# Kernel optimization log

Measured on AMD Instinct MI355X. Metric: run time of the kernel, lower is better.

Reference implementation:

```python
import jax, jax.numpy as jnp
import numpy as np

# Dimensions
B, T, S, V, CV, D = 32, 128, 400, 32000, 600, 512
PAD = 1  # vocabs['code'].stoi['<blank>']


def setup_inputs() -> dict:
    key = jax.random.key(0)
    k0, k1, k2, k3, k4 = jax.random.split(key, 5)
    hidden = jax.random.normal(k0, (B * T, D), dtype=jnp.float32)
    # attention weights: normalized over source length
    copy_attn = jax.nn.softmax(jax.random.normal(k1, (B * T, S), dtype=jnp.float32), axis=-1)
    # src_map: one-hot scatter matrix [B, S, CV] mapping src positions to extended-vocab ids
    src_ids = jax.random.randint(k2, (B, S), 0, CV)
    src_map = jax.nn.one_hot(src_ids, CV, dtype=jnp.float32)
    W = jax.random.normal(k3, (V, D), dtype=jnp.float32) * 0.02
    b = jnp.zeros((V,), dtype=jnp.float32)
    w_copy = jax.random.normal(k4, (D,), dtype=jnp.float32) * 0.02
    b_copy = jnp.zeros((), dtype=jnp.float32)
    return {"hidden": hidden, "copy_attn": copy_attn, "src_map": src_map,
            "W": W, "b": b, "w_copy": w_copy, "b_copy": b_copy}


def reference(hidden, copy_attn, src_map, W, b, w_copy, b_copy):
    # logits over target vocab, pad logit masked to -inf
    logits = hidden @ W.T + b                      # [B*T, V]
    logits = logits.at[:, PAD].set(-jnp.inf)
    prob = jax.nn.softmax(logits, axis=-1)         # [B*T, V]
    # copy gate p(z)
    copy = jax.nn.sigmoid(hidden @ w_copy + b_copy)[:, None]  # [B*T, 1]
    out_prob = prob * (1.0 - copy)                 # generation branch
    mul_attn = copy_attn * copy                    # copy branch, [B*T, S]
    # scatter attention mass into extended vocab via one-hot bmm
    copy_prob = jnp.einsum('bts,bsv->btv', mul_attn.reshape(B, T, S), src_map)
    copy_prob = copy_prob.reshape(-1, src_map.shape[-1])  # [B*T, CV]
    return jnp.concatenate([out_prob, copy_prob], axis=1)  # [B*T, V+CV]
```

## Files before the change

### kernel.cpp

```cpp
#include <hip/hip_runtime.h>
#include <hip/hip_bf16.h>
#include <cstdint>
#include <cstddef>

#define M_ROWS   4096
#define N_VOCAB  32000
#define K_DIM    512
#define S_DIM    400
#define CV_DIM   600
#define OUT_PITCH 32600
#define PAD_IDX  1

typedef __attribute__((ext_vector_type(8))) short short8;
typedef __attribute__((ext_vector_type(8))) unsigned short ushort8;
typedef __attribute__((ext_vector_type(4))) float f32x4;

#define WB_OFF   0ull
#define HB_OFF   32768000ull
#define COPYG_OFF 36962304ull
#define RSUM_OFF  36978688ull
#define SSCALE_OFF 36995072ull
#define SRCID_OFF 37011456ull
#define EB_OFF    37062656ull
#define WS_NEED_BF16 (EB_OFF + 262144000ull)

__device__ inline void gload_lds16(const void* g, void* l) {
  __builtin_amdgcn_global_load_lds(
      (const __attribute__((address_space(1))) unsigned int*)g,
      (__attribute__((address_space(3))) unsigned int*)l, 16, 0, 0);
}

__device__ inline unsigned short f32_to_bf16_rn(float f) {
  unsigned u = __float_as_uint(f);
  u += 0x7FFFu + ((u >> 16) & 1u);
  return (unsigned short)(u >> 16);
}
__device__ inline float bf16_to_f32(unsigned short h) {
  return __uint_as_float((unsigned)h << 16);
}

__global__ void cvt_kernel(const float4* __restrict__ in, ushort4* __restrict__ out, unsigned n4) {
  unsigned stride = gridDim.x * blockDim.x;
  for (unsigned i = blockIdx.x * blockDim.x + threadIdx.x; i < n4; i += stride) {
    float4 v = in[i];
    ushort4 o;
    o.x = f32_to_bf16_rn(v.x);
    o.y = f32_to_bf16_rn(v.y);
    o.z = f32_to_bf16_rn(v.z);
    o.w = f32_to_bf16_rn(v.w);
    out[i] = o;
  }
}

__global__ void copygate_kernel(const float* __restrict__ hidden, const float* __restrict__ w_copy,
                                const float* __restrict__ b_copy, float* __restrict__ copyg) {
  unsigned gw = (blockIdx.x * blockDim.x + threadIdx.x) >> 6;
  unsigned lane = threadIdx.x & 63u;
  if (gw >= M_ROWS) return;
  const float4* h4 = (const float4*)(hidden + (size_t)gw * K_DIM);
  const float4* w4 = (const float4*)w_copy;
  float dot = 0.f;
  #pragma unroll
  for (int i = 0; i < 2; ++i) {
    float4 a = h4[lane * 2 + i], w = w4[lane * 2 + i];
    dot += a.x * w.x + a.y * w.y + a.z * w.z + a.w * w.w;
  }
  #pragma unroll
  for (int mask = 1; mask < 64; mask <<= 1) dot += __shfl_xor(dot, mask);
  if (lane == 0) copyg[gw] = 1.f / (1.f + __expf(-(dot + b_copy[0])));
}

__global__ void srcids_kernel(const float* __restrict__ src_map, int* __restrict__ src_ids) {
  unsigned pos = (blockIdx.x * blockDim.x + threadIdx.x) >> 6;
  unsigned lane = threadIdx.x & 63u;
  if (pos >= 32 * S_DIM) return;
  const float* row = src_map + (size_t)pos * CV_DIM;
  int found = 1 << 30;
  for (int v = lane; v < CV_DIM; v += 64)
    if (row[v] > 0.5f) found = v;
  #pragma unroll
  for (int mask = 1; mask < 64; mask <<= 1) {
    int o = __shfl_xor(found, mask);
    found = found < o ? found : o;
  }
  if (lane == 0) src_ids[pos] = found;
}

template<int BF16OUT>
__global__ __launch_bounds__(256, 4)
void gemm_exp_kernel(const unsigned short* __restrict__ A,
                     const unsigned short* __restrict__ B,
                     const float* __restrict__ bias,
                     float* __restrict__ out,
                     unsigned short* __restrict__ Eb,
                     float* __restrict__ row_sum) {
  __shared__ unsigned short smem[16384];
  unsigned short* As = smem;
  unsigned short* Bs = smem + 8192;

  unsigned bid = blockIdx.x;
  unsigned wg = (bid & 7u) * 1000u + (bid >> 3);
  unsigned mt = wg / 250u, nt = wg % 250u;
  unsigned m0 = mt * 128u, n0 = nt * 128u;
  unsigned tid = threadIdx.x;
  unsigned lane = tid & 63u;
  unsigned wid = tid >> 6;
  unsigned wm = wid >> 1, wn = wid & 1u;
  unsigned lr = lane >> 4, lc = lane & 15u;

  const unsigned ch0 = (lr ^ (lc & 7u)) * 8u;
  const unsigned ch1 = ((lr + 4u) ^ (lc & 7u)) * 8u;

  const unsigned short* Asrc[4];
  const unsigned short* Bsrc[4];
  unsigned dst[4];
  #pragma unroll
  for (unsigned i = 0; i < 4; ++i) {
    unsigned u = i * 256u + tid;
    unsigned rr = u >> 3;
    unsigned ch = (u & 7u) ^ (rr & 7u);
    dst[i] = u * 16u;
    Asrc[i] = A + (size_t)(m0 + rr) * K_DIM + ch * 8u;
    Bsrc[i] = B + (size_t)(n0 + rr) * K_DIM + ch * 8u;
  }
  unsigned arow[4], brow[4];
  #pragma unroll
  for (int m = 0; m < 4; ++m) arow[m] = (wm * 64u + m * 16u + lc) * 64u;
  #pragma unroll
  for (int n = 0; n < 4; ++n) brow[n] = (wn * 64u + n * 16u + lc) * 64u;

  f32x4 acc[4][4] = {};

  for (unsigned kt = 0; kt < 8; ++kt) {
    unsigned k0 = kt * 64u;
    #pragma unroll
    for (unsigned i = 0; i < 4; ++i) {
      gload_lds16(Asrc[i] + k0, (char*)As + dst[i]);
      gload_lds16(Bsrc[i] + k0, (char*)Bs + dst[i]);
    }
    __syncthreads();
    {
      short8 af[4][2], bf[4][2];
      #pragma unroll
      for (int m = 0; m < 4; ++m) {
        af[m][0] = *(const short8*)&As[arow[m] + ch0];
        af[m][1] = *(const short8*)&As[arow[m] + ch1];
      }
      #pragma unroll
      for (int n = 0; n < 4; ++n) {
        bf[n][0] = *(const short8*)&Bs[brow[n] + ch0];
        bf[n][1] = *(const short8*)&Bs[brow[n] + ch1];
      }
      #pragma unroll
      for (int ks = 0; ks < 2; ++ks)
        #pragma unroll
        for (int m = 0; m < 4; ++m)
          #pragma unroll
          for (int n = 0; n < 4; ++n)
            acc[m][n] = __builtin_amdgcn_mfma_f32_16x16x32_bf16(af[m][ks], bf[n][ks],
                                                                acc[m][n], 0, 0, 0);
    }
    __syncthreads();
  }

  float bv[4];
  #pragma unroll
  for (int n = 0; n < 4; ++n) bv[n] = bias[n0 + wn * 64u + n * 16u + lc];

  if (BF16OUT) {
    #pragma unroll
    for (int m = 0; m < 4; ++m)
      #pragma unroll
      for (int j = 0; j < 4; ++j) {
        unsigned r = wm * 64u + m * 16u + lr * 4u + j;
        #pragma unroll
        for (int n = 0; n < 4; ++n) {
          unsigned c = wn * 64u + n * 16u + lc;
          unsigned gcol = n0 + c;
          float e = (gcol == PAD_IDX) ? 0.f : __expf(acc[m][n][j] + bv[n]);
          smem[r * 128u + (c ^ ((r & 7u) << 3))] = f32_to_bf16_rn(e);
        }
      }
    __syncthreads();
    {
      unsigned r = tid >> 1, c0 = (tid & 1u) * 64u;
      unsigned short* gdst = Eb + (size_t)(m0 + r) * N_VOCAB + n0 + c0;
      #pragma unroll
      for (unsigned q = 0; q < 8; ++q) {
        ushort8 v = *(const ushort8*)&smem[r * 128u + c0 + ((q ^ (r & 7u)) << 3)];
        *(ushort8*)(gdst + q * 8u) = v;
      }
    }
  } else {
    #pragma unroll
    for (int m = 0; m < 4; ++m) {
      #pragma unroll
      for (int j = 0; j < 4; ++j) {
        unsigned grow = m0 + wm * 64u + m * 16u + lr * 4u + j;
        float rs = 0.f;
        #pragma unroll
        for (int n = 0; n < 4; ++n) {
          unsigned gcol = n0 + wn * 64u + n * 16u + lc;
          float e = (gcol == PAD_IDX) ? 0.f : __expf(acc[m][n][j] + bv[n]);
          out[(size_t)grow * OUT_PITCH + gcol] = e;
          rs += e;
        }
        #pragma unroll
        for (int mask = 1; mask < 16; mask <<= 1) rs += __shfl_xor(rs, mask);
        if (lc == 0) atomicAdd(&row_sum[grow], rs);
      }
    }
  }
}

__global__ __launch_bounds__(256)
void norm_scale_kernel(const unsigned short* __restrict__ Eb,
                       const float* __restrict__ copyg,
                       float* __restrict__ out) {
  unsigned r = blockIdx.x;
  unsigned tid = threadIdx.x;
  const ushort8* src = (const ushort8*)(Eb + (size_t)r * N_VOCAB);
  ushort8 v[16];
  float lsum = 0.f;
  #pragma unroll
  for (int i = 0; i < 16; ++i) {
    unsigned c = (unsigned)i * 256u + tid;
    if (c < 4000u) {
      v[i] = src[c];
      #pragma unroll
      for (int k = 0; k < 8; ++k) lsum += bf16_to_f32(v[i][k]);
    }
  }
  #pragma unroll
  for (int mask = 1; mask < 64; mask <<= 1) lsum += __shfl_xor(lsum, mask);
  __shared__ float wsum[4];
  if ((tid & 63u) == 0) wsum[tid >> 6] = lsum;
  __syncthreads();
  float s = (1.f - copyg[r]) / (wsum[0] + wsum[1] + wsum[2] + wsum[3]);
  float* dst = out + (size_t)r * OUT_PITCH;
  #pragma unroll
  for (int i = 0; i < 16; ++i) {
    unsigned c = (unsigned)i * 256u + tid;
    if (c < 4000u) {
      float4 lo, hi;
      lo.x = bf16_to_f32(v[i][0]) * s; lo.y = bf16_to_f32(v[i][1]) * s;
      lo.z = bf16_to_f32(v[i][2]) * s; lo.w = bf16_to_f32(v[i][3]) * s;
      hi.x = bf16_to_f32(v[i][4]) * s; hi.y = bf16_to_f32(v[i][5]) * s;
      hi.z = bf16_to_f32(v[i][6]) * s; hi.w = bf16_to_f32(v[i][7]) * s;
      float4* o = (float4*)(dst + c * 8u);
      o[0] = lo; o[1] = hi;
    }
  }
}

__global__ void finalize_kernel(const float* __restrict__ row_sum, const float* __restrict__ copyg,
                                float* __restrict__ sscale) {
  unsigned r = blockIdx.x * blockDim.x + threadIdx.x;
  if (r < M_ROWS) sscale[r] = (1.f - copyg[r]) / row_sum[r];
}

__global__ void scale_kernel(float4* __restrict__ out, const float* __restrict__ sscale) {
  const unsigned total = M_ROWS * (N_VOCAB / 4);
  unsigned stride = gridDim.x * blockDim.x;
  for (unsigned i = blockIdx.x * blockDim.x + threadIdx.x; i < total; i += stride) {
    unsigned r = i / (N_VOCAB / 4);
    unsigned c = i % (N_VOCAB / 4);
    float s = sscale[r];
    float4 v = out[(size_t)r * (OUT_PITCH / 4) + c];
    v.x *= s; v.y *= s; v.z *= s; v.w *= s;
    out[(size_t)r * (OUT_PITCH / 4) + c] = v;
  }
}

__global__ void copyprob_kernel(const float* __restrict__ attn, const int* __restrict__ src_ids,
                                const float* __restrict__ copyg, float* __restrict__ out) {
  unsigned r = blockIdx.x;
  unsigned tid = threadIdx.x;
  __shared__ float cp[CV_DIM];
  for (unsigned v = tid; v < CV_DIM; v += 128) cp[v] = 0.f;
  __syncthreads();
  unsigned batch = r >> 7;
  float g = copyg[r];
  for (unsigned s = tid; s < S_DIM; s += 128) {
    float a = attn[(size_t)r * S_DIM + s] * g;
    atomicAdd(&cp[src_ids[batch * S_DIM + s]], a);
  }
  __syncthreads();
  for (unsigned v = tid; v < CV_DIM; v += 128)
    out[(size_t)r * OUT_PITCH + N_VOCAB + v] = cp[v];
}

extern "C" void kernel_launch(void* const* d_in, const int* in_sizes, int n_in,
                              void* d_out, int out_size, void* d_ws, size_t ws_size,
                              hipStream_t stream) {
  const float* hidden    = (const float*)d_in[0];
  const float* copy_attn = (const float*)d_in[1];
  const float* src_map   = (const float*)d_in[2];
  const float* W         = (const float*)d_in[3];
  const float* bias      = (const float*)d_in[4];
  const float* w_copy    = (const float*)d_in[5];
  const float* b_copy    = (const float*)d_in[6];
  float* out = (float*)d_out;

  char* ws = (char*)d_ws;
  unsigned short* Wb = (unsigned short*)(ws + WB_OFF);
  unsigned short* Hb = (unsigned short*)(ws + HB_OFF);
  float* copyg   = (float*)(ws + COPYG_OFF);
  float* row_sum = (float*)(ws + RSUM_OFF);
  float* sscale  = (float*)(ws + SSCALE_OFF);
  int*   src_ids = (int*)(ws + SRCID_OFF);
  unsigned short* Eb = (unsigned short*)(ws + EB_OFF);

  const bool bf16_path = (ws_size >= WS_NEED_BF16);

  cvt_kernel<<<2048, 256, 0, stream>>>((const float4*)W, (ushort4*)Wb,
                                       (unsigned)(N_VOCAB * K_DIM / 4));
  cvt_kernel<<<1024, 256, 0, stream>>>((const float4*)hidden, (ushort4*)Hb,
                                       (unsigned)(M_ROWS * K_DIM / 4));
  copygate_kernel<<<M_ROWS / 4, 256, 0, stream>>>(hidden, w_copy, b_copy, copyg);
  srcids_kernel<<<(32 * S_DIM) / 4, 256, 0, stream>>>(src_map, src_ids);

  if (bf16_path) {
    gemm_exp_kernel<1><<<(M_ROWS / 128) * (N_VOCAB / 128), 256, 0, stream>>>(
        Hb, Wb, bias, out, Eb, row_sum);
    norm_scale_kernel<<<M_ROWS, 256, 0, stream>>>(Eb, copyg, out);
  } else {
    hipMemsetAsync(row_sum, 0, M_ROWS * sizeof(float), stream);
    gemm_exp_kernel<0><<<(M_ROWS / 128) * (N_VOCAB / 128), 256, 0, stream>>>(
        Hb, Wb, bias, out, Eb, row_sum);
    finalize_kernel<<<(M_ROWS + 255) / 256, 256, 0, stream>>>(row_sum, copyg, sscale);
    scale_kernel<<<4096, 256, 0, stream>>>((float4*)out, sscale);
  }

  copyprob_kernel<<<M_ROWS, 128, 0, stream>>>(copy_attn, src_ids, copyg, out);
}
```

Before: 431.3 us.

## Double-buffer GEMM K-loop with 32-wide K tiles and async prefetch

Rewrites the GEMM main loop to use two LDS buffers of 32-wide K tiles, so the global-to-LDS load for the next tile is issued before computing on the current one. Uses explicit vmcnt waits and raw s_barrier instead of __syncthreads, and adds a new XOR swizzle for the 4-chunk rows. This is meant to hide global load latency behind MFMA work. In exchange it runs twice as many loop iterations with more barriers, and its correctness depends on the manual waitcnt counts.

```diff
diff --git a/kernel.cpp b/kernel.cpp
--- a/kernel.cpp
+++ b/kernel.cpp
@@ -95,8 +95,6 @@
                      unsigned short* __restrict__ Eb,
                      float* __restrict__ row_sum) {
   __shared__ unsigned short smem[16384];
-  unsigned short* As = smem;
-  unsigned short* Bs = smem + 8192;
 
   unsigned bid = blockIdx.x;
   unsigned wg = (bid & 7u) * 1000u + (bid >> 3);
@@ -108,59 +106,66 @@
   unsigned wm = wid >> 1, wn = wid & 1u;
   unsigned lr = lane >> 4, lc = lane & 15u;
 
-  const unsigned ch0 = (lr ^ (lc & 7u)) * 8u;
-  const unsigned ch1 = ((lr + 4u) ^ (lc & 7u)) * 8u;
-
-  const unsigned short* Asrc[4];
-  const unsigned short* Bsrc[4];
-  unsigned dst[4];
-  #pragma unroll
-  for (unsigned i = 0; i < 4; ++i) {
+  const unsigned ch = lr ^ (lc & 3u) ^ ((lc >> 2) & 3u);
+
+  const unsigned short* AsrcP[2];
+  const unsigned short* BsrcP[2];
+  unsigned dstB[2];
+  #pragma unroll
+  for (unsigned i = 0; i < 2; ++i) {
     unsigned u = i * 256u + tid;
-    unsigned rr = u >> 3;
-    unsigned ch = (u & 7u) ^ (rr & 7u);
-    dst[i] = u * 16u;
-    Asrc[i] = A + (size_t)(m0 + rr) * K_DIM + ch * 8u;
-    Bsrc[i] = B + (size_t)(n0 + rr) * K_DIM + ch * 8u;
-  }
-  unsigned arow[4], brow[4];
-  #pragma unroll
-  for (int m = 0; m < 4; ++m) arow[m] = (wm * 64u + m * 16u + lc) * 64u;
-  #pragma unroll
-  for (int n = 0; n < 4; ++n) brow[n] = (wn * 64u + n * 16u + lc) * 64u;
+    unsigned r = u >> 2, c = u & 3u;
+    unsigned cs = c ^ (r & 3u) ^ ((r >> 2) & 3u);
+    dstB[i] = u * 16u;
+    AsrcP[i] = A + (size_t)(m0 + r) * K_DIM + cs * 8u;
+    BsrcP[i] = B + (size_t)(n0 + r) * K_DIM + cs * 8u;
+  }
+  unsigned aidx[4], bidx[4];
+  #pragma unroll
+  for (int m = 0; m < 4; ++m) aidx[m] = (wm * 64u + m * 16u + lc) * 32u + ch * 8u;
+  #pragma unroll
+  for (int n = 0; n < 4; ++n) bidx[n] = 4096u + (wn * 64u + n * 16u + lc) * 32u + ch * 8u;
+
+  auto STAGE = [&](unsigned buf, unsigned kt) {
+    unsigned k0 = kt * 32u;
+    char* base = (char*)smem + buf * 16384u;
+    #pragma unroll
+    for (unsigned i = 0; i < 2; ++i) {
+      gload_lds16(AsrcP[i] + k0, base + dstB[i]);
+      gload_lds16(BsrcP[i] + k0, base + 8192u + dstB[i]);
+    }
+  };
 
   f32x4 acc[4][4] = {};
 
-  for (unsigned kt = 0; kt < 8; ++kt) {
-    unsigned k0 = kt * 64u;
-    #pragma unroll
-    for (unsigned i = 0; i < 4; ++i) {
-      gload_lds16(Asrc[i] + k0, (char*)As + dst[i]);
-      gload_lds16(Bsrc[i] + k0, (char*)Bs + dst[i]);
-    }
-    __syncthreads();
+  STAGE(0, 0);
+  #pragma unroll 4
+  for (int kt = 0; kt < 16; ++kt) {
+    unsigned bufo = ((unsigned)kt & 1u) * 8192u;
+    if (kt < 15) {
+      STAGE((unsigned)(kt + 1) & 1u, (unsigned)kt + 1u);
+      asm volatile("s_waitcnt vmcnt(4)" ::: "memory");
+    } else {
+      asm volatile("s_waitcnt vmcnt(0)" ::: "memory");
+    }
+    __builtin_amdgcn_s_barrier();
+    asm volatile("" ::: "memory");
+    __builtin_amdgcn_sched_barrier(0);
     {
-      short8 af[4][2], bf[4][2];
-      #pragma unroll
-      for (int m = 0; m < 4; ++m) {
-        af[m][0] = *(const short8*)&As[arow[m] + ch0];
-        af[m][1] = *(const short8*)&As[arow[m] + ch1];
-      }
-      #pragma unroll
-      for (int n = 0; n < 4; ++n) {
-        bf[n][0] = *(const short8*)&Bs[brow[n] + ch0];
-        bf[n][1] = *(const short8*)&Bs[brow[n] + ch1];
-      }
-      #pragma unroll
-      for (int ks = 0; ks < 2; ++ks)
+      short8 af[4], bf[4];
+      #pragma unroll
+      for (int m = 0; m < 4; ++m) af[m] = *(const short8*)&smem[bufo + aidx[m]];
+      #pragma unroll
+      for (int n = 0; n < 4; ++n) bf[n] = *(const short8*)&smem[bufo + bidx[n]];
+      #pragma unroll
+      for (int m = 0; m < 4; ++m)
         #pragma unroll
-        for (int m = 0; m < 4; ++m)
-          #pragma unroll
-          for (int n = 0; n < 4; ++n)
-            acc[m][n] = __builtin_amdgcn_mfma_f32_16x16x32_bf16(af[m][ks], bf[n][ks],
-                                                                acc[m][n], 0, 0, 0);
-    }
-    __syncthreads();
+        for (int n = 0; n < 4; ++n)
+          acc[m][n] = __builtin_amdgcn_mfma_f32_16x16x32_bf16(af[m], bf[n],
+                                                              acc[m][n], 0, 0, 0);
+    }
+    __builtin_amdgcn_s_barrier();
+    asm volatile("" ::: "memory");
   }
 
   float bv[4];
```

Result: slower. 443.5 us (+2.8%).
